# Performance work log

Hardware: AMD Instinct MI355X
Metric: run time of the kernel (lower is better)

Reference implementation:

```python
import jax, jax.numpy as jnp
import numpy as np
from jax import lax

B, C, L = 4, 64, 4096
EPS = 1e-5  # BatchNorm1d default eps


def setup_inputs() -> dict:
    key = jax.random.key(0)
    ks = jax.random.split(key, 10)
    s_conv = 1.0 / np.sqrt(C * 3)
    s_1x1 = 1.0 / np.sqrt(C)
    return {
        "x": jax.random.normal(ks[0], (B, C, L), jnp.float32),
        "conv_w": jax.random.uniform(ks[1], (C, C, 3), jnp.float32, -s_conv, s_conv),
        "conv_b": jax.random.uniform(ks[2], (C,), jnp.float32, -s_conv, s_conv),
        "wq": jax.random.uniform(ks[3], (C, C), jnp.float32, -s_1x1, s_1x1),
        "bq": jax.random.uniform(ks[4], (C,), jnp.float32, -s_1x1, s_1x1),
        "wk": jax.random.uniform(ks[5], (C, C), jnp.float32, -s_1x1, s_1x1),
        "bk": jax.random.uniform(ks[6], (C,), jnp.float32, -s_1x1, s_1x1),
        "wv": jax.random.uniform(ks[7], (C, C), jnp.float32, -s_1x1, s_1x1),
        "bv": jax.random.uniform(ks[8], (C,), jnp.float32, -s_1x1, s_1x1),
        "gamma": jnp.ones((C,), jnp.float32),
        "beta": jnp.zeros((C,), jnp.float32),
    }


def reference(x, conv_w, conv_b, wq, bq, wk, bk, wv, bv, gamma, beta):
    residual = x
    h = jax.nn.elu(x)
    # circular padding for kernel-3 conv (padding=1, padding_mode='circular')
    hp = jnp.concatenate([h[:, :, -1:], h, h[:, :, :1]], axis=-1)  # [B,C,L+2]
    h = lax.conv_general_dilated(
        hp, conv_w, window_strides=(1,), padding="VALID",
        dimension_numbers=("NCH", "OIH", "NCH"),
    ) + conv_b[None, :, None]  # [B,C,L]
    # QKV 1x1 convs == per-position linear over channels
    q = jnp.einsum("oc,bcl->bol", wq, h) + bq[None, :, None]
    k = jnp.einsum("oc,bcl->bol", wk, h) + bk[None, :, None]
    v = jnp.einsum("oc,bcl->bol", wv, h) + bv[None, :, None]
    # SpatialGate: cm = q^T k [B,L,L]; out = v @ cm [B,C,L] (no softmax)
    cm = jnp.einsum("bcl,bcm->blm", q, k)
    g = jnp.einsum("bcl,blm->bcm", v, cm)
    y = g + residual
    # BatchNorm1d in training mode: per-channel stats over (B, L), biased var
    mean = jnp.mean(y, axis=(0, 2), keepdims=True)
    var = jnp.mean((y - mean) ** 2, axis=(0, 2), keepdims=True)
    out = gamma[None, :, None] * (y - mean) * lax.rsqrt(var + EPS) + beta[None, :, None]
    return out
```

## Files before the change

kernel.cpp:

```cpp
#include <hip/hip_runtime.h>
#include <math.h>

#define LDIM 4096
#define CDIM 64
#define NB 4
#define TL 64
#define NBLK (LDIM / TL)
#define NBLOCKS (NB * NBLK)
#define EPS 1e-5f
#define XS 68

#define K_OFF 0
#define Y_OFF (NB * CDIM * LDIM)
#define P_OFF (2 * NB * CDIM * LDIM)
#define M_OFF (P_OFF + NBLOCKS * CDIM * CDIM)
#define CW_OFF (M_OFF + NB * CDIM * CDIM)
#define SP_OFF (CW_OFF + 16 * CDIM * 16)
#define S_OFF (SP_OFF + NBLOCKS * 2 * CDIM)

__device__ __forceinline__ float elu1(float t) { return t > 0.f ? t : expm1f(t); }

__global__ __launch_bounds__(256) void k_prep(
    const float* __restrict__ cw, float* __restrict__ cwT)
{
    int idx = blockIdx.x * 256 + threadIdx.x;
    int t  = idx & 3;
    int di = (idx >> 2) & 3;
    int c  = (idx >> 4) & 63;
    int i4 = idx >> 10;
    float v = (t < 3) ? cw[(c * CDIM + i4 * 4 + di) * 3 + t] : 0.f;
    cwT[idx] = v;
}

__global__ __launch_bounds__(1024, 4) void k_front(
    const float* __restrict__ x,
    const float* __restrict__ cwT, const float* __restrict__ conv_b,
    const float* __restrict__ wq, const float* __restrict__ bq,
    const float* __restrict__ wk, const float* __restrict__ bk,
    const float* __restrict__ wv, const float* __restrict__ bv,
    float* __restrict__ k_ws, float* __restrict__ P_ws)
{
    __shared__ alignas(16) float xe[CDIM][XS];
    __shared__ alignas(16) float hs[CDIM][XS];
    __shared__ alignas(16) float qsT[TL][XS];
    __shared__ alignas(16) float vsT[TL][XS];

    const int b   = blockIdx.y;
    const int l0  = blockIdx.x * TL;
    const int tid = threadIdx.x;
    const int c   = tid >> 4;
    const int p0  = (tid & 15) << 2;

    const float* xb = x + (size_t)b * CDIM * LDIM;

    {
        float4 xv = *reinterpret_cast<const float4*>(xb + (size_t)c * LDIM + l0 + p0);
        xe[c][p0 + 1] = elu1(xv.x);
        xe[c][p0 + 2] = elu1(xv.y);
        xe[c][p0 + 3] = elu1(xv.z);
        xe[c][p0 + 4] = elu1(xv.w);
        if (tid < CDIM)
            xe[tid][0] = elu1(xb[(size_t)tid * LDIM + ((l0 - 1) & (LDIM - 1))]);
        else if (tid < 2 * CDIM)
            xe[tid - CDIM][TL + 1] =
                elu1(xb[(size_t)(tid - CDIM) * LDIM + ((l0 + TL) & (LDIM - 1))]);
    }
    __syncthreads();

    const float4* cw4 = (const float4*)cwT;
    float hacc[4];
    {
        float cb = conv_b[c];
        hacc[0] = hacc[1] = hacc[2] = hacc[3] = cb;
    }
    for (int i4 = 0; i4 < 16; ++i4) {
        float4 w[4];
#pragma unroll
        for (int di = 0; di < 4; ++di)
            w[di] = cw4[(size_t)(i4 * 64 + c) * 4 + di];
#pragma unroll
        for (int di = 0; di < 4; ++di) {
            const float* xr = &xe[i4 * 4 + di][p0];
            float4 a  = *reinterpret_cast<const float4*>(xr);
            float2 e2 = *reinterpret_cast<const float2*>(xr + 4);
            hacc[0] = fmaf(w[di].x, a.x, fmaf(w[di].y, a.y, fmaf(w[di].z, a.z,  hacc[0])));
            hacc[1] = fmaf(w[di].x, a.y, fmaf(w[di].y, a.z, fmaf(w[di].z, a.w,  hacc[1])));
            hacc[2] = fmaf(w[di].x, a.z, fmaf(w[di].y, a.w, fmaf(w[di].z, e2.x, hacc[2])));
            hacc[3] = fmaf(w[di].x, a.w, fmaf(w[di].y, e2.x, fmaf(w[di].z, e2.y, hacc[3])));
        }
    }
    *reinterpret_cast<float4*>(&hs[c][p0]) =
        make_float4(hacc[0], hacc[1], hacc[2], hacc[3]);
    __syncthreads();

    const float4* wq4 = (const float4*)wq;
    const float4* wk4 = (const float4*)wk;
    const float4* wv4 = (const float4*)wv;
    float qa[4], ka[4], va[4];
    {
        float t;
        t = bq[c]; qa[0] = qa[1] = qa[2] = qa[3] = t;
        t = bk[c]; ka[0] = ka[1] = ka[2] = ka[3] = t;
        t = bv[c]; va[0] = va[1] = va[2] = va[3] = t;
    }
    for (int i4 = 0; i4 < 16; ++i4) {
        float4 aq = wq4[c * 16 + i4];
        float4 ak = wk4[c * 16 + i4];
        float4 av = wv4[c * 16 + i4];
        float4 h0 = *reinterpret_cast<const float4*>(&hs[i4 * 4 + 0][p0]);
        float4 h1 = *reinterpret_cast<const float4*>(&hs[i4 * 4 + 1][p0]);
        float4 h2 = *reinterpret_cast<const float4*>(&hs[i4 * 4 + 2][p0]);
        float4 h3 = *reinterpret_cast<const float4*>(&hs[i4 * 4 + 3][p0]);
        qa[0] = fmaf(aq.x, h0.x, fmaf(aq.y, h1.x, fmaf(aq.z, h2.x, fmaf(aq.w, h3.x, qa[0]))));
        qa[1] = fmaf(aq.x, h0.y, fmaf(aq.y, h1.y, fmaf(aq.z, h2.y, fmaf(aq.w, h3.y, qa[1]))));
        qa[2] = fmaf(aq.x, h0.z, fmaf(aq.y, h1.z, fmaf(aq.z, h2.z, fmaf(aq.w, h3.z, qa[2]))));
        qa[3] = fmaf(aq.x, h0.w, fmaf(aq.y, h1.w, fmaf(aq.z, h2.w, fmaf(aq.w, h3.w, qa[3]))));
        ka[0] = fmaf(ak.x, h0.x, fmaf(ak.y, h1.x, fmaf(ak.z, h2.x, fmaf(ak.w, h3.x, ka[0]))));
        ka[1] = fmaf(ak.x, h0.y, fmaf(ak.y, h1.y, fmaf(ak.z, h2.y, fmaf(ak.w, h3.y, ka[1]))));
        ka[2] = fmaf(ak.x, h0.z, fmaf(ak.y, h1.z, fmaf(ak.z, h2.z, fmaf(ak.w, h3.z, ka[2]))));
        ka[3] = fmaf(ak.x, h0.w, fmaf(ak.y, h1.w, fmaf(ak.z, h2.w, fmaf(ak.w, h3.w, ka[3]))));
        va[0] = fmaf(av.x, h0.x, fmaf(av.y, h1.x, fmaf(av.z, h2.x, fmaf(av.w, h3.x, va[0]))));
        va[1] = fmaf(av.x, h0.y, fmaf(av.y, h1.y, fmaf(av.z, h2.y, fmaf(av.w, h3.y, va[1]))));
        va[2] = fmaf(av.x, h0.z, fmaf(av.y, h1.z, fmaf(av.z, h2.z, fmaf(av.w, h3.z, va[2]))));
        va[3] = fmaf(av.x, h0.w, fmaf(av.y, h1.w, fmaf(av.z, h2.w, fmaf(av.w, h3.w, va[3]))));
    }
    *reinterpret_cast<float4*>(k_ws + ((size_t)b * CDIM + c) * LDIM + l0 + p0) =
        make_float4(ka[0], ka[1], ka[2], ka[3]);
    qsT[p0 + 0][c] = qa[0]; qsT[p0 + 1][c] = qa[1];
    qsT[p0 + 2][c] = qa[2]; qsT[p0 + 3][c] = qa[3];
    vsT[p0 + 0][c] = va[0]; vsT[p0 + 1][c] = va[1];
    vsT[p0 + 2][c] = va[2]; vsT[p0 + 3][c] = va[3];
    __syncthreads();

    const int cv  = tid >> 4;
    const int cq0 = (tid & 15) * 4;
    float m0 = 0.f, m1 = 0.f, m2 = 0.f, m3 = 0.f;
    for (int l = 0; l < TL; ++l) {
        const float  vv = vsT[l][cv];
        const float4 qq = *reinterpret_cast<const float4*>(&qsT[l][cq0]);
        m0 = fmaf(vv, qq.x, m0);
        m1 = fmaf(vv, qq.y, m1);
        m2 = fmaf(vv, qq.z, m2);
        m3 = fmaf(vv, qq.w, m3);
    }
    float4* Pb = (float4*)(P_ws + ((size_t)b * NBLK + blockIdx.x) * CDIM * CDIM);
    Pb[cv * (CDIM / 4) + (cq0 >> 2)] = make_float4(m0, m1, m2, m3);
}

__global__ __launch_bounds__(256) void k_reduceM(
    const float* __restrict__ P_ws, float* __restrict__ M_ws)
{
    const int b  = blockIdx.x >> 2;
    const int e4 = (blockIdx.x & 3) * 256 + threadIdx.x;
    const float4* Pf4 = (const float4*)P_ws + (size_t)b * NBLK * (CDIM * CDIM / 4);
    float4 s0 = make_float4(0, 0, 0, 0), s1 = s0, s2 = s0, s3 = s0;
    for (int blk = 0; blk < NBLK; blk += 4) {
        float4 p0 = Pf4[(size_t)(blk + 0) * (CDIM * CDIM / 4) + e4];
        float4 p1 = Pf4[(size_t)(blk + 1) * (CDIM * CDIM / 4) + e4];
        float4 p2 = Pf4[(size_t)(blk + 2) * (CDIM * CDIM / 4) + e4];
        float4 p3 = Pf4[(size_t)(blk + 3) * (CDIM * CDIM / 4) + e4];
        s0.x += p0.x; s0.y += p0.y; s0.z += p0.z; s0.w += p0.w;
        s1.x += p1.x; s1.y += p1.y; s1.z += p1.z; s1.w += p1.w;
        s2.x += p2.x; s2.y += p2.y; s2.z += p2.z; s2.w += p2.w;
        s3.x += p3.x; s3.y += p3.y; s3.z += p3.z; s3.w += p3.w;
    }
    float4 s = make_float4((s0.x + s1.x) + (s2.x + s3.x),
                           (s0.y + s1.y) + (s2.y + s3.y),
                           (s0.z + s1.z) + (s2.z + s3.z),
                           (s0.w + s1.w) + (s2.w + s3.w));
    ((float4*)M_ws)[(size_t)b * (CDIM * CDIM / 4) + e4] = s;
}

__global__ __launch_bounds__(1024, 4) void k_spatial(
    const float* __restrict__ x, const float* __restrict__ k_ws,
    const float* __restrict__ M_ws, float* __restrict__ y_ws,
    float* __restrict__ spB)
{
    __shared__ alignas(16) float kl[CDIM][XS];
    __shared__ alignas(16) float Ms[CDIM][XS];
    const int b   = blockIdx.y;
    const int l0  = blockIdx.x * TL;
    const int tid = threadIdx.x;
    const int c   = tid >> 4;
    const int p0  = (tid & 15) << 2;

    *reinterpret_cast<float4*>(&Ms[c][p0]) =
        ((const float4*)M_ws)[(size_t)b * (CDIM * CDIM / 4) + tid];
    *reinterpret_cast<float4*>(&kl[c][p0]) =
        *reinterpret_cast<const float4*>(k_ws + ((size_t)b * CDIM + c) * LDIM + l0 + p0);
    __syncthreads();

    float4 acc = *reinterpret_cast<const float4*>(
        x + ((size_t)b * CDIM + c) * LDIM + l0 + p0);
    for (int i4 = 0; i4 < 16; ++i4) {
        float4 mv = *reinterpret_cast<const float4*>(&Ms[c][i4 * 4]);
        float4 k0 = *reinterpret_cast<const float4*>(&kl[i4 * 4 + 0][p0]);
        float4 k1 = *reinterpret_cast<const float4*>(&kl[i4 * 4 + 1][p0]);
        float4 k2 = *reinterpret_cast<const float4*>(&kl[i4 * 4 + 2][p0]);
        float4 k3 = *reinterpret_cast<const float4*>(&kl[i4 * 4 + 3][p0]);
        acc.x = fmaf(mv.x, k0.x, fmaf(mv.y, k1.x, fmaf(mv.z, k2.x, fmaf(mv.w, k3.x, acc.x))));
        acc.y = fmaf(mv.x, k0.y, fmaf(mv.y, k1.y, fmaf(mv.z, k2.y, fmaf(mv.w, k3.y, acc.y))));
        acc.z = fmaf(mv.x, k0.z, fmaf(mv.y, k1.z, fmaf(mv.z, k2.z, fmaf(mv.w, k3.z, acc.z))));
        acc.w = fmaf(mv.x, k0.w, fmaf(mv.y, k1.w, fmaf(mv.z, k2.w, fmaf(mv.w, k3.w, acc.w))));
    }
    *reinterpret_cast<float4*>(y_ws + ((size_t)b * CDIM + c) * LDIM + l0 + p0) = acc;

    const int blk = blockIdx.y * NBLK + blockIdx.x;
    float s  = (acc.x + acc.y) + (acc.z + acc.w);
    float s2 = fmaf(acc.x, acc.x, fmaf(acc.y, acc.y,
               fmaf(acc.z, acc.z, acc.w * acc.w)));
    for (int off = 8; off; off >>= 1) {
        s  += __shfl_down(s, off);
        s2 += __shfl_down(s2, off);
    }
    if ((tid & 15) == 0) {
        spB[(size_t)blk * (2 * CDIM) + c] = s;
        spB[(size_t)blk * (2 * CDIM) + CDIM + c] = s2;
    }
}

__global__ __launch_bounds__(512) void k_reduceS(
    const float* __restrict__ spB, float* __restrict__ sums)
{
    __shared__ float red[4][128];
    const int t = threadIdx.x & 127;
    const int q = threadIdx.x >> 7;
    float s0 = 0.f, s1 = 0.f, s2 = 0.f, s3 = 0.f;
    const int r0 = q * 64;
    for (int r = r0; r < r0 + 64; r += 4) {
        s0 += spB[(r + 0) * (2 * CDIM) + t];
        s1 += spB[(r + 1) * (2 * CDIM) + t];
        s2 += spB[(r + 2) * (2 * CDIM) + t];
        s3 += spB[(r + 3) * (2 * CDIM) + t];
    }
    red[q][t] = (s0 + s1) + (s2 + s3);
    __syncthreads();
    if (threadIdx.x < 128)
        sums[t] = (red[0][t] + red[1][t]) + (red[2][t] + red[3][t]);
}

__global__ __launch_bounds__(256) void k_norm(
    const float* __restrict__ y_ws, const float* __restrict__ sums,
    const float* __restrict__ gamma, const float* __restrict__ beta,
    float* __restrict__ out)
{
    const int idx = blockIdx.x * 256 + threadIdx.x;
    const int c   = (idx >> 10) & (CDIM - 1);
    const float inv = 1.f / (float)(NB * LDIM);
    float s    = sums[c];
    float s2   = sums[CDIM + c];
    float mean = s * inv;
    float var  = fmaf(-mean, mean, s2 * inv);
    float rstd = 1.f / sqrtf(var + EPS);
    float g    = gamma[c] * rstd;
    float bb   = fmaf(-mean, g, beta[c]);

    float4 v = ((const float4*)y_ws)[idx];
    float4 o;
    o.x = fmaf(v.x, g, bb);
    o.y = fmaf(v.y, g, bb);
    o.z = fmaf(v.z, g, bb);
    o.w = fmaf(v.w, g, bb);
    ((float4*)out)[idx] = o;
}

extern "C" void kernel_launch(void* const* d_in, const int* in_sizes, int n_in,
                              void* d_out, int out_size, void* d_ws, size_t ws_size,
                              hipStream_t stream)
{
    const float* x      = (const float*)d_in[0];
    const float* conv_w = (const float*)d_in[1];
    const float* conv_b = (const float*)d_in[2];
    const float* wq     = (const float*)d_in[3];
    const float* bq     = (const float*)d_in[4];
    const float* wk     = (const float*)d_in[5];
    const float* bk     = (const float*)d_in[6];
    const float* wv     = (const float*)d_in[7];
    const float* bv     = (const float*)d_in[8];
    const float* gamma  = (const float*)d_in[9];
    const float* beta   = (const float*)d_in[10];

    float* ws   = (float*)d_ws;
    float* k_ws = ws + K_OFF;
    float* y_ws = ws + Y_OFF;
    float* P_ws = ws + P_OFF;
    float* M_ws = ws + M_OFF;
    float* cwT  = ws + CW_OFF;
    float* spB  = ws + SP_OFF;
    float* sums = ws + S_OFF;

    dim3 grid(NBLK, NB);
    k_prep<<<64, 256, 0, stream>>>(conv_w, cwT);
    k_front<<<grid, 1024, 0, stream>>>(x, cwT, conv_b, wq, bq, wk, bk,
                                       wv, bv, k_ws, P_ws);
    k_reduceM<<<16, 256, 0, stream>>>(P_ws, M_ws);
    k_spatial<<<grid, 1024, 0, stream>>>(x, k_ws, M_ws, y_ws, spB);
    k_reduceS<<<1, 512, 0, stream>>>(spB, sums);

    const int n4 = NB * CDIM * LDIM / 4;
    k_norm<<<n4 / 256, 256, 0, stream>>>(y_ws, sums, gamma, beta, (float*)d_out);
}
```

Measured before the change: 123.1 us.

## Fuse spatial, stats reduction and BatchNorm into one cooperative kernel

Replaces the k_spatial, k_reduceS and k_norm launches with a single cooperative kernel that computes y, writes per-block partial stats, does a grid-wide sync, reduces the stats redundantly in every block and writes the normalized output straight from registers. This avoids writing y to a workspace and reading it back, and removes two launches. It also drops the k_prep weight-transpose kernel by reading conv_w directly in k_front, and adds unroll-2 pragmas. The grid sync needs all 256 blocks of 1024 threads to be co-resident, and there is a fallback to the old path if the cooperative launch fails.

```diff
diff --git a/kernel.cpp b/kernel.cpp
--- a/kernel.cpp
+++ b/kernel.cpp
@@ -1,5 +1,8 @@
 #include <hip/hip_runtime.h>
+#include <hip/hip_cooperative_groups.h>
 #include <math.h>
+
+namespace cg = cooperative_groups;
 
 #define LDIM 4096
 #define CDIM 64
@@ -14,27 +17,14 @@
 #define Y_OFF (NB * CDIM * LDIM)
 #define P_OFF (2 * NB * CDIM * LDIM)
 #define M_OFF (P_OFF + NBLOCKS * CDIM * CDIM)
-#define CW_OFF (M_OFF + NB * CDIM * CDIM)
-#define SP_OFF (CW_OFF + 16 * CDIM * 16)
+#define SP_OFF (M_OFF + NB * CDIM * CDIM)
 #define S_OFF (SP_OFF + NBLOCKS * 2 * CDIM)
 
 __device__ __forceinline__ float elu1(float t) { return t > 0.f ? t : expm1f(t); }
-
-__global__ __launch_bounds__(256) void k_prep(
-    const float* __restrict__ cw, float* __restrict__ cwT)
-{
-    int idx = blockIdx.x * 256 + threadIdx.x;
-    int t  = idx & 3;
-    int di = (idx >> 2) & 3;
-    int c  = (idx >> 4) & 63;
-    int i4 = idx >> 10;
-    float v = (t < 3) ? cw[(c * CDIM + i4 * 4 + di) * 3 + t] : 0.f;
-    cwT[idx] = v;
-}
 
 __global__ __launch_bounds__(1024, 4) void k_front(
     const float* __restrict__ x,
-    const float* __restrict__ cwT, const float* __restrict__ conv_b,
+    const float* __restrict__ conv_w, const float* __restrict__ conv_b,
     const float* __restrict__ wq, const float* __restrict__ bq,
     const float* __restrict__ wk, const float* __restrict__ bk,
     const float* __restrict__ wv, const float* __restrict__ bv,
@@ -67,26 +57,29 @@
     }
     __syncthreads();
 
-    const float4* cw4 = (const float4*)cwT;
     float hacc[4];
     {
         float cb = conv_b[c];
         hacc[0] = hacc[1] = hacc[2] = hacc[3] = cb;
     }
+#pragma unroll 2
     for (int i4 = 0; i4 < 16; ++i4) {
-        float4 w[4];
-#pragma unroll
-        for (int di = 0; di < 4; ++di)
-            w[di] = cw4[(size_t)(i4 * 64 + c) * 4 + di];
+        const float4* wrow = (const float4*)(conv_w + (size_t)c * 192 + i4 * 12);
+        float4 f0 = wrow[0], f1 = wrow[1], f2 = wrow[2];
+        float wx[4], wy[4], wz[4];
+        wx[0] = f0.x; wy[0] = f0.y; wz[0] = f0.z;
+        wx[1] = f0.w; wy[1] = f1.x; wz[1] = f1.y;
+        wx[2] = f1.z; wy[2] = f1.w; wz[2] = f2.x;
+        wx[3] = f2.y; wy[3] = f2.z; wz[3] = f2.w;
 #pragma unroll
         for (int di = 0; di < 4; ++di) {
             const float* xr = &xe[i4 * 4 + di][p0];
             float4 a  = *reinterpret_cast<const float4*>(xr);
             float2 e2 = *reinterpret_cast<const float2*>(xr + 4);
-            hacc[0] = fmaf(w[di].x, a.x, fmaf(w[di].y, a.y, fmaf(w[di].z, a.z,  hacc[0])));
-            hacc[1] = fmaf(w[di].x, a.y, fmaf(w[di].y, a.z, fmaf(w[di].z, a.w,  hacc[1])));
-            hacc[2] = fmaf(w[di].x, a.z, fmaf(w[di].y, a.w, fmaf(w[di].z, e2.x, hacc[2])));
-            hacc[3] = fmaf(w[di].x, a.w, fmaf(w[di].y, e2.x, fmaf(w[di].z, e2.y, hacc[3])));
+            hacc[0] = fmaf(wx[di], a.x, fmaf(wy[di], a.y, fmaf(wz[di], a.z,  hacc[0])));
+            hacc[1] = fmaf(wx[di], a.y, fmaf(wy[di], a.z, fmaf(wz[di], a.w,  hacc[1])));
+            hacc[2] = fmaf(wx[di], a.z, fmaf(wy[di], a.w, fmaf(wz[di], e2.x, hacc[2])));
+            hacc[3] = fmaf(wx[di], a.w, fmaf(wy[di], e2.x, fmaf(wz[di], e2.y, hacc[3])));
         }
     }
     *reinterpret_cast<float4*>(&hs[c][p0]) =
@@ -103,6 +96,7 @@
         t = bk[c]; ka[0] = ka[1] = ka[2] = ka[3] = t;
         t = bv[c]; va[0] = va[1] = va[2] = va[3] = t;
     }
+#pragma unroll 2
     for (int i4 = 0; i4 < 16; ++i4) {
         float4 aq = wq4[c * 16 + i4];
         float4 ak = wk4[c * 16 + i4];
@@ -171,6 +165,94 @@
     ((float4*)M_ws)[(size_t)b * (CDIM * CDIM / 4) + e4] = s;
 }
 
+__global__ __launch_bounds__(1024, 4) void k_back(
+    const float* __restrict__ x, const float* __restrict__ k_ws,
+    const float* __restrict__ M_ws, const float* __restrict__ gamma,
+    const float* __restrict__ beta, float* __restrict__ spB,
+    float* __restrict__ out)
+{
+    __shared__ alignas(16) float kl[CDIM][XS];
+    __shared__ alignas(16) float Ms[CDIM][XS];
+    __shared__ float red[8][128];
+    __shared__ float sums2[2 * CDIM];
+
+    const int b   = blockIdx.y;
+    const int l0  = blockIdx.x * TL;
+    const int tid = threadIdx.x;
+    const int c   = tid >> 4;
+    const int p0  = (tid & 15) << 2;
+
+    *reinterpret_cast<float4*>(&Ms[c][p0]) =
+        ((const float4*)M_ws)[(size_t)b * (CDIM * CDIM / 4) + tid];
+    *reinterpret_cast<float4*>(&kl[c][p0]) =
+        *reinterpret_cast<const float4*>(k_ws + ((size_t)b * CDIM + c) * LDIM + l0 + p0);
+    __syncthreads();
+
+    float4 acc = *reinterpret_cast<const float4*>(
+        x + ((size_t)b * CDIM + c) * LDIM + l0 + p0);
+#pragma unroll 2
+    for (int i4 = 0; i4 < 16; ++i4) {
+        float4 mv = *reinterpret_cast<const float4*>(&Ms[c][i4 * 4]);
+        float4 k0 = *reinterpret_cast<const float4*>(&kl[i4 * 4 + 0][p0]);
+        float4 k1 = *reinterpret_cast<const float4*>(&kl[i4 * 4 + 1][p0]);
+        float4 k2 = *reinterpret_cast<const float4*>(&kl[i4 * 4 + 2][p0]);
+        float4 k3 = *reinterpret_cast<const float4*>(&kl[i4 * 4 + 3][p0]);
+        acc.x = fmaf(mv.x, k0.x, fmaf(mv.y, k1.x, fmaf(mv.z, k2.x, fmaf(mv.w, k3.x, acc.x))));
+        acc.y = fmaf(mv.x, k0.y, fmaf(mv.y, k1.y, fmaf(mv.z, k2.y, fmaf(mv.w, k3.y, acc.y))));
+        acc.z = fmaf(mv.x, k0.z, fmaf(mv.y, k1.z, fmaf(mv.z, k2.z, fmaf(mv.w, k3.z, acc.z))));
+        acc.w = fmaf(mv.x, k0.w, fmaf(mv.y, k1.w, fmaf(mv.z, k2.w, fmaf(mv.w, k3.w, acc.w))));
+    }
+
+    const int blk = blockIdx.y * NBLK + blockIdx.x;
+    {
+        float s  = (acc.x + acc.y) + (acc.z + acc.w);
+        float s2 = fmaf(acc.x, acc.x, fmaf(acc.y, acc.y,
+                   fmaf(acc.z, acc.z, acc.w * acc.w)));
+        for (int off = 8; off; off >>= 1) {
+            s  += __shfl_down(s, off);
+            s2 += __shfl_down(s2, off);
+        }
+        if ((tid & 15) == 0) {
+            spB[(size_t)blk * (2 * CDIM) + c] = s;
+            spB[(size_t)blk * (2 * CDIM) + CDIM + c] = s2;
+        }
+    }
+    __threadfence();
+    cg::this_grid().sync();
+
+    {
+        const int t = tid & 127;
+        const int g = tid >> 7;
+        float s0 = 0.f, s1 = 0.f;
+        const int r0 = g * 32;
+        for (int r = r0; r < r0 + 32; r += 2) {
+            s0 += spB[(size_t)(r + 0) * (2 * CDIM) + t];
+            s1 += spB[(size_t)(r + 1) * (2 * CDIM) + t];
+        }
+        red[g][t] = s0 + s1;
+    }
+    __syncthreads();
+    if (tid < 128) {
+        const int t = tid;
+        sums2[t] = ((red[0][t] + red[1][t]) + (red[2][t] + red[3][t]))
+                 + ((red[4][t] + red[5][t]) + (red[6][t] + red[7][t]));
+    }
+    __syncthreads();
+
+    const float inv = 1.f / (float)(NB * LDIM);
+    float mean = sums2[c] * inv;
+    float var  = fmaf(-mean, mean, sums2[CDIM + c] * inv);
+    float rstd = 1.f / sqrtf(var + EPS);
+    float g    = gamma[c] * rstd;
+    float bb   = fmaf(-mean, g, beta[c]);
+    float4 o;
+    o.x = fmaf(acc.x, g, bb);
+    o.y = fmaf(acc.y, g, bb);
+    o.z = fmaf(acc.z, g, bb);
+    o.w = fmaf(acc.w, g, bb);
+    *reinterpret_cast<float4*>(out + ((size_t)b * CDIM + c) * LDIM + l0 + p0) = o;
+}
+
 __global__ __launch_bounds__(1024, 4) void k_spatial(
     const float* __restrict__ x, const float* __restrict__ k_ws,
     const float* __restrict__ M_ws, float* __restrict__ y_ws,
@@ -285,18 +367,23 @@
     float* y_ws = ws + Y_OFF;
     float* P_ws = ws + P_OFF;
     float* M_ws = ws + M_OFF;
-    float* cwT  = ws + CW_OFF;
     float* spB  = ws + SP_OFF;
     float* sums = ws + S_OFF;
+    float* outp = (float*)d_out;
 
     dim3 grid(NBLK, NB);
-    k_prep<<<64, 256, 0, stream>>>(conv_w, cwT);
-    k_front<<<grid, 1024, 0, stream>>>(x, cwT, conv_b, wq, bq, wk, bk,
+    k_front<<<grid, 1024, 0, stream>>>(x, conv_w, conv_b, wq, bq, wk, bk,
                                        wv, bv, k_ws, P_ws);
     k_reduceM<<<16, 256, 0, stream>>>(P_ws, M_ws);
-    k_spatial<<<grid, 1024, 0, stream>>>(x, k_ws, M_ws, y_ws, spB);
-    k_reduceS<<<1, 512, 0, stream>>>(spB, sums);
-
-    const int n4 = NB * CDIM * LDIM / 4;
-    k_norm<<<n4 / 256, 256, 0, stream>>>(y_ws, sums, gamma, beta, (float*)d_out);
-}
+
+    void* args[] = {(void*)&x, (void*)&k_ws, (void*)&M_ws, (void*)&gamma,
+                    (void*)&beta, (void*)&spB, (void*)&outp};
+    hipError_t err = hipLaunchCooperativeKernel(
+        reinterpret_cast<void*>(k_back), grid, dim3(1024), args, 0, stream);
+    if (err != hipSuccess) {
+        k_spatial<<<grid, 1024, 0, stream>>>(x, k_ws, M_ws, y_ws, spB);
+        k_reduceS<<<1, 512, 0, stream>>>(spB, sums);
+        const int n4 = NB * CDIM * LDIM / 4;
+        k_norm<<<n4 / 256, 256, 0, stream>>>(y_ws, sums, gamma, beta, outp);
+    }
+}
```

Result: slower. 224.6 us (+82.5%).
